# Performance work log

Hardware: AMD Instinct MI355X
Metric: run time of the kernel (lower is better)

Reference implementation:

```python
import jax, jax.numpy as jnp
import numpy as np

B, C_IN, C_OUT, H, W = 16, 32, 32, 256, 256
M1, M2 = 32, 32  # kept Fourier modes (kbase // 2**level)


def setup_inputs() -> dict:
    key = jax.random.key(0)
    ks = jax.random.split(key, 7)
    scale = 1.0 / (C_IN * C_OUT)
    return {
        "x": jax.random.normal(ks[0], (B, C_IN, H, W), dtype=jnp.float32),
        "conv_w": jax.random.normal(ks[1], (C_OUT, 3 * C_IN), dtype=jnp.float32) * (1.0 / np.sqrt(3 * C_IN)),
        "conv_b": jax.random.normal(ks[2], (C_OUT,), dtype=jnp.float32) * 0.01,
        "w1r": jax.random.normal(ks[3], (C_IN, C_OUT, M1, M2), dtype=jnp.float32) * scale,
        "w1i": jax.random.normal(ks[4], (C_IN, C_OUT, M1, M2), dtype=jnp.float32) * scale,
        "w2r": jax.random.normal(ks[5], (C_IN, C_OUT, M1, M2), dtype=jnp.float32) * scale,
        "w2i": jax.random.normal(ks[6], (C_IN, C_OUT, M1, M2), dtype=jnp.float32) * scale,
    }


def _combi_forward(x, conv_w, conv_b, w1r, w1i, w2r, w2i):
    # ---- diff branch: EasyDiffs (x, forward-diff along H, forward-diff along W) + 1x1 conv ----
    zrow = jnp.zeros_like(x[:, :, :1, :])
    zcol = jnp.zeros_like(x[:, :, :, :1])
    dh = jnp.concatenate([x[:, :, 1:, :] - x[:, :, :-1, :], zrow], axis=2)  # [B,C,H,W]
    dw = jnp.concatenate([x[:, :, :, 1:] - x[:, :, :, :-1], zcol], axis=3)  # [B,C,H,W]
    feats = jnp.concatenate([x, dh, dw], axis=1)  # [B,3C,H,W]
    diff_out = jnp.einsum("bchw,oc->bohw", feats, conv_w) + conv_b[None, :, None, None]

    # ---- spectral branch: rfft2 -> truncated complex multiply (two corners) -> irfft2 ----
    xf = jnp.fft.rfft2(x, axes=(-2, -1))  # [B,C,H,W//2+1] complex
    w1 = w1r + 1j * w1i
    w2 = w2r + 1j * w2i
    top = jnp.einsum("bixy,ioxy->boxy", xf[:, :, :M1, :M2], w1)
    bot = jnp.einsum("bixy,ioxy->boxy", xf[:, :, -M1:, :M2], w2)
    out_ft = jnp.zeros((B, C_OUT, H, W // 2 + 1), dtype=xf.dtype)
    out_ft = out_ft.at[:, :, :M1, :M2].set(top)
    out_ft = out_ft.at[:, :, -M1:, :M2].set(bot)
    fno_out = jnp.fft.irfft2(out_ft, s=(H, W), axes=(-2, -1))

    return diff_out + fno_out


def reference(x, conv_w, conv_b, w1r, w1i, w2r, w2i):
    return _combi_forward(x, conv_w, conv_b, w1r, w1i, w2r, w2i)
```

## Files before the change

### kernel.cpp

```cpp
#include <hip/hip_runtime.h>


#define PI2_256 0.02454369260617026f

__device__ __forceinline__ unsigned short bf16r(float f) {
    unsigned u = __float_as_uint(f);
    u += 0x7fffu + ((u >> 16) & 1u);
    return (unsigned short)(u >> 16);
}
__device__ __forceinline__ float bf16tof(unsigned short h) {
    return __uint_as_float((unsigned)h << 16);
}
__device__ __forceinline__ unsigned pack2(float a, float b) {
    return (unsigned)bf16r(a) | ((unsigned)bf16r(b) << 16);
}

typedef __attribute__((ext_vector_type(8))) short short8;
typedef __attribute__((ext_vector_type(4))) float float4v;

__global__ __launch_bounds__(256) void k_twiddle(float* __restrict__ ws) {
    unsigned short* E = (unsigned short*)(ws + 8388608);
    int idx0 = blockIdx.x * 256 + threadIdx.x;
    for (int idx = idx0; idx < 4 * 64 * 72; idx += 16 * 256) {
        int c = idx / 4608;
        int rem = idx - c * 4608;
        int col = rem / 72;
        int wp = rem - col * 72;
        unsigned short hi = 0, lo = 0;
        if (wp < 64) {
            int w = c * 64 + wp;
            int ky = col & 31;
            int prod = (ky * w) & 255;
            float s, cc;
            __sincosf(PI2_256 * (float)prod, &s, &cc);
            float val = (col < 32) ? cc : -s;
            hi = bf16r(val);
            lo = bf16r(val - bf16tof(hi));
        }
        E[c * 9216 + col * 72 + wp] = hi;
        E[c * 9216 + 4608 + col * 72 + wp] = lo;
    }
}

__global__ __launch_bounds__(256) void k_dftw(const float* __restrict__ x,
                                              const float* __restrict__ Ews,
                                              float* __restrict__ Ar,
                                              float* __restrict__ Ai) {
    __shared__ __align__(16) unsigned char smem[55296];
    unsigned short* Xhi = (unsigned short*)smem;
    unsigned short* Xlo = (unsigned short*)(smem + 18432);
    unsigned short* Ehi = (unsigned short*)(smem + 36864);
    float* obuf = (float*)smem;

    int t = threadIdx.x;
    int bc = blockIdx.x >> 1;
    int h0 = (blockIdx.x & 1) << 7;
    int lane = t & 63, wid = t >> 6;
    int quad = lane >> 4, col = lane & 15;

    const uint4* Ews4 = (const uint4*)Ews;

    float4v zero = {0.f, 0.f, 0.f, 0.f};
    float4v acc[4][2];
#pragma unroll
    for (int m = 0; m < 4; ++m) {
        acc[m][0] = zero;
        acc[m][1] = zero;
    }

    for (int c = 0; c < 4; ++c) {
        const float* xrow = x + ((size_t)bc * 256 + h0) * 256 + c * 64;
#pragma unroll
        for (int it = 0; it < 8; ++it) {
            int l = it * 256 + t;
            int r = l >> 4, f4 = l & 15;
            float4 v = *(const float4*)(xrow + (size_t)r * 256 + f4 * 4);
            unsigned short hx = bf16r(v.x), hy = bf16r(v.y);
            unsigned short hz = bf16r(v.z), hw = bf16r(v.w);
            unsigned hi0 = (unsigned)hx | ((unsigned)hy << 16);
            unsigned hi1 = (unsigned)hz | ((unsigned)hw << 16);
            unsigned lo0 = (unsigned)bf16r(v.x - bf16tof(hx)) |
                           ((unsigned)bf16r(v.y - bf16tof(hy)) << 16);
            unsigned lo1 = (unsigned)bf16r(v.z - bf16tof(hz)) |
                           ((unsigned)bf16r(v.w - bf16tof(hw)) << 16);
            int o = r * 72 + f4 * 4;
            *(uint2*)&Xhi[o] = make_uint2(hi0, hi1);
            *(uint2*)&Xlo[o] = make_uint2(lo0, lo1);
        }
        for (int g = t; g < 1152; g += 256)
            ((uint4*)(smem + 36864))[g] = Ews4[c * 1152 + g];
        __syncthreads();

#pragma unroll
        for (int ks = 0; ks < 2; ++ks) {
            int ko = quad * 8 + ks * 32;
            short8 ah[4], al[4], bh[2], bl[2];
#pragma unroll
            for (int m = 0; m < 4; ++m) {
                int ro = (m * 16 + col) * 72 + ko;
                ah[m] = *(const short8*)&Ehi[ro];
                al[m] = *(const short8*)&Ehi[4608 + ro];
            }
#pragma unroll
            for (int n = 0; n < 2; ++n) {
                int hr = ((wid * 2 + n) * 16 + col) * 72 + ko;
                bh[n] = *(const short8*)&Xhi[hr];
                bl[n] = *(const short8*)&Xlo[hr];
            }
#pragma unroll
            for (int m = 0; m < 4; ++m) {
#pragma unroll
                for (int n = 0; n < 2; ++n) {
                    acc[m][n] = __builtin_amdgcn_mfma_f32_16x16x32_bf16(ah[m], bh[n], acc[m][n], 0, 0, 0);
                    acc[m][n] = __builtin_amdgcn_mfma_f32_16x16x32_bf16(ah[m], bl[n], acc[m][n], 0, 0, 0);
                    acc[m][n] = __builtin_amdgcn_mfma_f32_16x16x32_bf16(al[m], bh[n], acc[m][n], 0, 0, 0);
                }
            }
        }
        __syncthreads();
    }

#pragma unroll
    for (int m = 0; m < 4; ++m) {
#pragma unroll
        for (int n = 0; n < 2; ++n) {
            int hl = (wid * 2 + n) * 16 + col;
            *(float4v*)&obuf[hl * 68 + m * 16 + quad * 4] = acc[m][n];
        }
    }
    __syncthreads();
#pragma unroll
    for (int it = 0; it < 8; ++it) {
        int l = it * 256 + t;
        int hh = l >> 4, f = l & 15;
        float4 v = *(float4*)&obuf[hh * 68 + f * 4];
        size_t g = (size_t)bc * 8192 + (size_t)(h0 + hh) * 32;
        if (f < 8) *(float4*)(Ar + g + f * 4) = v;
        else       *(float4*)(Ai + g + (f - 8) * 4) = v;
    }
}

#define DF_PITCH 72

__global__ __launch_bounds__(256) void k_dfth(const float* __restrict__ Ar,
                                              const float* __restrict__ Ai,
                                              float* __restrict__ xfr,
                                              float* __restrict__ xfi) {
    __shared__ __align__(16) unsigned short F2h[128 * DF_PITCH];
    __shared__ __align__(16) unsigned short F2l[128 * DF_PITCH];
    __shared__ __align__(16) unsigned short B2h[32 * DF_PITCH];
    __shared__ __align__(16) unsigned short B2l[32 * DF_PITCH];

    int t = threadIdx.x;
    int bc = blockIdx.x;
    int lane = t & 63, wid = t >> 6;
    int quad = lane >> 4, col = lane & 15;

    int m = t & 127;
    int kxi = m >> 1;
    int kx = (kxi < 32) ? kxi : kxi + 192;
    int neg = m & 1;
    int khalf = t >> 7;
    float c1, s1;
    __sincosf(PI2_256 * (float)kx, &s1, &c1);

    float4v zero = {0.f, 0.f, 0.f, 0.f};
    float4v acc[2][2];
    acc[0][0] = zero; acc[0][1] = zero; acc[1][0] = zero; acc[1][1] = zero;

    for (int hc = 0; hc < 8; ++hc) {
        {
            int h0 = hc * 32 + khalf * 16;
            float c, s;
            __sincosf(PI2_256 * (float)((kx * h0) & 255), &s, &c);
#pragma unroll
            for (int j = 0; j < 16; ++j) {
                int kk = 2 * (khalf * 16 + j);
                float ch = bf16tof(bf16r(c)), sh = bf16tof(bf16r(s));
                float cl = c - ch, sl = s - sh;
                unsigned hiw, low;
                if (neg == 0) { hiw = pack2(c, s);  low = pack2(cl, sl); }
                else          { hiw = pack2(-s, c); low = pack2(-sl, cl); }
                *(unsigned*)&F2h[m * DF_PITCH + kk] = hiw;
                *(unsigned*)&F2l[m * DF_PITCH + kk] = low;
                float nc = c * c1 - s * s1;
                s = s * c1 + c * s1;
                c = nc;
            }
        }
        {
            int hl = t >> 3;
            int ky0 = (t & 7) * 4;
            const float* pr = Ar + (size_t)bc * 8192 + (size_t)(hc * 32 + hl) * 32 + ky0;
            const float* pi = Ai + (size_t)bc * 8192 + (size_t)(hc * 32 + hl) * 32 + ky0;
            float4 vr = *(const float4*)pr;
            float4 vi = *(const float4*)pi;
            float fr[4] = {vr.x, vr.y, vr.z, vr.w};
            float fi[4] = {vi.x, vi.y, vi.z, vi.w};
#pragma unroll
            for (int q = 0; q < 4; ++q) {
                float ar = fr[q], ai = fi[q];
                float arh = bf16tof(bf16r(ar)), aih = bf16tof(bf16r(ai));
                *(unsigned*)&B2h[(ky0 + q) * DF_PITCH + 2 * hl] = pack2(ar, ai);
                *(unsigned*)&B2l[(ky0 + q) * DF_PITCH + 2 * hl] = pack2(ar - arh, ai - aih);
            }
        }
        __syncthreads();
#pragma unroll
        for (int ks = 0; ks < 2; ++ks) {
            int ko = ks * 32 + quad * 8;
            short8 ah[2], al[2], bh[2], bl[2];
#pragma unroll
            for (int mi = 0; mi < 2; ++mi) {
                int ro = ((wid * 2 + mi) * 16 + col) * DF_PITCH + ko;
                ah[mi] = *(const short8*)&F2h[ro];
                al[mi] = *(const short8*)&F2l[ro];
            }
#pragma unroll
            for (int ni = 0; ni < 2; ++ni) {
                int ro = (ni * 16 + col) * DF_PITCH + ko;
                bh[ni] = *(const short8*)&B2h[ro];
                bl[ni] = *(const short8*)&B2l[ro];
            }
#pragma unroll
            for (int mi = 0; mi < 2; ++mi) {
#pragma unroll
                for (int ni = 0; ni < 2; ++ni) {
                    acc[mi][ni] = __builtin_amdgcn_mfma_f32_16x16x32_bf16(ah[mi], bh[ni], acc[mi][ni], 0, 0, 0);
                    acc[mi][ni] = __builtin_amdgcn_mfma_f32_16x16x32_bf16(ah[mi], bl[ni], acc[mi][ni], 0, 0, 0);
                    acc[mi][ni] = __builtin_amdgcn_mfma_f32_16x16x32_bf16(al[mi], bh[ni], acc[mi][ni], 0, 0, 0);
                }
            }
        }
        __syncthreads();
    }
#pragma unroll
    for (int mi = 0; mi < 2; ++mi) {
#pragma unroll
        for (int ni = 0; ni < 2; ++ni) {
#pragma unroll
            for (int reg = 0; reg < 4; ++reg) {
                int mm = (wid * 2 + mi) * 16 + quad * 4 + reg;
                size_t g = (size_t)bc * 2048 + (size_t)(mm >> 1) * 32 + ni * 16 + col;
                if (mm & 1) xfi[g] = acc[mi][ni][reg];
                else        xfr[g] = acc[mi][ni][reg];
            }
        }
    }
}

__global__ __launch_bounds__(256) void k_mix(float* __restrict__ xfr,
                                             float* __restrict__ xfi,
                                             const float* __restrict__ w1r,
                                             const float* __restrict__ w1i,
                                             const float* __restrict__ w2r,
                                             const float* __restrict__ w2i) {
    __shared__ float wr[32 * 32 * 8];
    __shared__ float wi[32 * 32 * 8];
    __shared__ float xsr[32 * 8];
    __shared__ float xsi[32 * 8];
    int t = threadIdx.x;
    int kxi = (blockIdx.x >> 2) & 63;
    int ky0 = (blockIdx.x & 3) * 8;
    int b0 = (blockIdx.x >> 8) * 4;
    const float* Wr = (kxi < 32) ? w1r : w2r;
    const float* Wi = (kxi < 32) ? w1i : w2i;
    int m1 = kxi & 31;
#pragma unroll
    for (int it = 0; it < 32; ++it) {
        int l = it * 256 + t;
        int i = l >> 8, o = (l >> 3) & 31, q = l & 7;
        size_t g = (size_t)i * 32768 + (size_t)o * 1024 + m1 * 32 + ky0 + q;
        wr[l] = Wr[g];
        wi[l] = Wi[g];
    }
    __syncthreads();

    int o = t >> 3, q = t & 7;
    for (int b = b0; b < b0 + 4; ++b) {
        __syncthreads();
        {
            int i = t >> 3, qq = t & 7;
            size_t g = ((size_t)(b * 32 + i)) * 2048 + (size_t)kxi * 32 + ky0 + qq;
            xsr[t] = xfr[g];
            xsi[t] = xfi[g];
        }
        __syncthreads();
        float accr = 0.f, acci = 0.f;
#pragma unroll
        for (int i = 0; i < 32; ++i) {
            float xr = xsr[i * 8 + q], xim = xsi[i * 8 + q];
            float wrv = wr[i * 256 + o * 8 + q], wiv = wi[i * 256 + o * 8 + q];
            accr += xr * wrv - xim * wiv;
            acci += xr * wiv + xim * wrv;
        }
        size_t g = ((size_t)(b * 32 + o)) * 2048 + (size_t)kxi * 32 + ky0 + q;
        xfr[g] = accr;
        xfi[g] = acci;
    }
}

#define IF_PITCH 136

__global__ __launch_bounds__(256) void k_idfth(const float* __restrict__ ofr,
                                               const float* __restrict__ ofi,
                                               float* __restrict__ T) {
    __shared__ __align__(16) unsigned short Fh[64 * IF_PITCH];
    __shared__ __align__(16) unsigned short Fl[64 * IF_PITCH];
    __shared__ __align__(16) unsigned short Gh[64 * IF_PITCH];
    __shared__ __align__(16) unsigned short Gl[64 * IF_PITCH];

    int t = threadIdx.x;
    int bo = blockIdx.x;
    int lane = t & 63, wid = t >> 6;
    int quad = lane >> 4, col = lane & 15;

    {
        int kxi = t >> 2;
        int ky0 = (t & 3) * 8;
        const float* pr = ofr + (size_t)bo * 2048 + (size_t)kxi * 32 + ky0;
        const float* pi = ofi + (size_t)bo * 2048 + (size_t)kxi * 32 + ky0;
        float4 r0 = *(const float4*)pr, r1 = *(const float4*)(pr + 4);
        float4 i0 = *(const float4*)pi, i1 = *(const float4*)(pi + 4);
        float fr[8] = {r0.x, r0.y, r0.z, r0.w, r1.x, r1.y, r1.z, r1.w};
        float fi[8] = {i0.x, i0.y, i0.z, i0.w, i1.x, i1.y, i1.z, i1.w};
#pragma unroll
        for (int q = 0; q < 8; ++q) {
            int ky = ky0 + q;
            float sc = ((ky == 0) ? 1.f : 2.f) * (1.f / 65536.f);
            float vr = fr[q] * sc, vi = fi[q] * sc;
            float vrh = bf16tof(bf16r(vr)), vih = bf16tof(bf16r(vi));
            float vrl = vr - vrh, vil = vi - vih;
            *(unsigned*)&Gh[(2 * ky) * IF_PITCH + 2 * kxi]     = pack2(vr, -vi);
            *(unsigned*)&Gh[(2 * ky + 1) * IF_PITCH + 2 * kxi] = pack2(vi, vr);
            *(unsigned*)&Gl[(2 * ky) * IF_PITCH + 2 * kxi]     = pack2(vrl, -vil);
            *(unsigned*)&Gl[(2 * ky + 1) * IF_PITCH + 2 * kxi] = pack2(vil, vrl);
        }
    }

    int hl_ = t & 63;
    int g = t >> 6;
    int kxi0 = g * 16;
    int kx0 = (g < 2) ? kxi0 : kxi0 + 192;

    for (int hc = 0; hc < 4; ++hc) {
        int h = hc * 64 + hl_;
        {
            float c1, s1;
            __sincosf(PI2_256 * (float)h, &s1, &c1);
            float c, s;
            __sincosf(PI2_256 * (float)((kx0 * h) & 255), &s, &c);
#pragma unroll
            for (int j = 0; j < 16; ++j) {
                int kk = 2 * (kxi0 + j);
                float ch = bf16tof(bf16r(c)), sh = bf16tof(bf16r(s));
                *(unsigned*)&Fh[hl_ * IF_PITCH + kk] = pack2(c, s);
                *(unsigned*)&Fl[hl_ * IF_PITCH + kk] = pack2(c - ch, s - sh);
                float nc = c * c1 - s * s1;
                s = s * c1 + c * s1;
                c = nc;
            }
        }
        __syncthreads();
        float4v zero = {0.f, 0.f, 0.f, 0.f};
        float4v acc[4];
        acc[0] = zero; acc[1] = zero; acc[2] = zero; acc[3] = zero;
#pragma unroll
        for (int ks = 0; ks < 4; ++ks) {
            int ko = ks * 32 + quad * 8;
            short8 bh = *(const short8*)&Gh[(wid * 16 + col) * IF_PITCH + ko];
            short8 bl = *(const short8*)&Gl[(wid * 16 + col) * IF_PITCH + ko];
#pragma unroll
            for (int mt = 0; mt < 4; ++mt) {
                int ro = (mt * 16 + col) * IF_PITCH + ko;
                short8 ah = *(const short8*)&Fh[ro];
                short8 al = *(const short8*)&Fl[ro];
                acc[mt] = __builtin_amdgcn_mfma_f32_16x16x32_bf16(ah, bh, acc[mt], 0, 0, 0);
                acc[mt] = __builtin_amdgcn_mfma_f32_16x16x32_bf16(ah, bl, acc[mt], 0, 0, 0);
                acc[mt] = __builtin_amdgcn_mfma_f32_16x16x32_bf16(al, bh, acc[mt], 0, 0, 0);
            }
        }
        float* dst = T + (size_t)bo * 16384 + (size_t)hc * 4096;
#pragma unroll
        for (int mt = 0; mt < 4; ++mt) {
#pragma unroll
            for (int reg = 0; reg < 4; ++reg) {
                int hh = mt * 16 + quad * 4 + reg;
                dst[hh * 64 + wid * 16 + col] = acc[mt][reg];
            }
        }
        __syncthreads();
    }
}

#define BT_PITCH 164

__global__ __launch_bounds__(256) void k_final(const float* __restrict__ x,
                                               const float* __restrict__ cw,
                                               const float* __restrict__ cb,
                                               const float* __restrict__ T,
                                               float* __restrict__ out) {
    __shared__ unsigned short Bt[128 * BT_PITCH];
    __shared__ __align__(16) unsigned short Afr[5 * 2 * 64 * 8];

    int t = threadIdx.x;
    int b = blockIdx.x >> 9;
    int h = (blockIdx.x >> 1) & 255;
    int w0 = (blockIdx.x & 1) << 7;

    {
        int nn = t & 127, half = t >> 7;
        int w = w0 + nn;
        int hs = (h < 255) ? h + 1 : h;
        int we = (w < 255) ? 1 : 0;
#pragma unroll
        for (int ip = 0; ip < 8; ++ip) {
            int i0 = half * 16 + ip * 2;
            const float* x0 = x + ((size_t)(b * 32 + i0)) * 65536;
            const float* x1 = x0 + 65536;
            float c0 = x0[h * 256 + w];
            float s0 = x0[hs * 256 + w];
            float e0 = x0[h * 256 + w + we];
            float c1 = x1[h * 256 + w];
            float s1 = x1[hs * 256 + w];
            float e1 = x1[h * 256 + w + we];
            *(unsigned*)&Bt[nn * BT_PITCH + i0]      = pack2(c0, c1);
            *(unsigned*)&Bt[nn * BT_PITCH + 32 + i0] = pack2(s0 - c0, s1 - c1);
            *(unsigned*)&Bt[nn * BT_PITCH + 64 + i0] = pack2(e0 - c0, e1 - c1);
        }
    }
    {
        int nn = t & 127, half = t >> 7;
        int w = w0 + nn;
        float c1, s1;
        __sincosf(PI2_256 * (float)w, &s1, &c1);
        int kk0 = half * 16;
        float c, s;
        __sincosf(PI2_256 * (float)((w * kk0) & 255), &s, &c);
#pragma unroll
        for (int kp = 0; kp < 8; ++kp) {
            int kk = kk0 + kp * 2;
            float ca = c, sa = s;
            float nc = c * c1 - s * s1; s = s * c1 + c * s1; c = nc;
            float cbv = c, sbv = s;
            nc = c * c1 - s * s1; s = s * c1 + c * s1; c = nc;
            *(unsigned*)&Bt[nn * BT_PITCH + 96 + kk]  = pack2(ca, cbv);
            *(unsigned*)&Bt[nn * BT_PITCH + 128 + kk] = pack2(-sa, -sbv);
        }
    }
    for (int slot = t; slot < 640; slot += 256) {
        int ks = slot >> 7;
        int mt = (slot >> 6) & 1;
        int lane = slot & 63;
        int m = (lane & 15) + mt * 16;
        int kb = ks * 32 + (lane >> 4) * 8;
        float v[8];
        if (ks < 3) {
#pragma unroll
            for (int j = 0; j < 8; ++j) v[j] = cw[m * 96 + kb + j];
        } else {
            const float* tp = T + ((size_t)(b * 32 + m)) * 16384 + (size_t)h * 64;
            int kkb = kb - (ks == 3 ? 96 : 128);
            int im = (ks == 3) ? 0 : 1;
#pragma unroll
            for (int j = 0; j < 8; ++j) v[j] = tp[2 * (kkb + j) + im];
        }
        uint4 pk;
        pk.x = pack2(v[0], v[1]); pk.y = pack2(v[2], v[3]);
        pk.z = pack2(v[4], v[5]); pk.w = pack2(v[6], v[7]);
        *(uint4*)&Afr[((ks * 2 + mt) * 64 + lane) * 8] = pk;
    }
    __syncthreads();

    int lane = t & 63, wid = t >> 6;
    int quad = lane >> 4, col = lane & 15;
    float4v zero = {0.f, 0.f, 0.f, 0.f};
    float4v acc[2][2];
    acc[0][0] = zero; acc[0][1] = zero; acc[1][0] = zero; acc[1][1] = zero;

#pragma unroll
    for (int ks = 0; ks < 5; ++ks) {
        short8 a0 = *(const short8*)&Afr[((ks * 2 + 0) * 64 + lane) * 8];
        short8 a1 = *(const short8*)&Afr[((ks * 2 + 1) * 64 + lane) * 8];
        int kb = ks * 32 + quad * 8;
        union { unsigned long long q[2]; short8 v; } ub0, ub1;
        const unsigned short* r0 = &Bt[(wid * 32 + col) * BT_PITCH + kb];
        const unsigned short* r1 = &Bt[(wid * 32 + 16 + col) * BT_PITCH + kb];
        ub0.q[0] = *(const unsigned long long*)(r0);
        ub0.q[1] = *(const unsigned long long*)(r0 + 4);
        ub1.q[0] = *(const unsigned long long*)(r1);
        ub1.q[1] = *(const unsigned long long*)(r1 + 4);
        acc[0][0] = __builtin_amdgcn_mfma_f32_16x16x32_bf16(a0, ub0.v, acc[0][0], 0, 0, 0);
        acc[1][0] = __builtin_amdgcn_mfma_f32_16x16x32_bf16(a1, ub0.v, acc[1][0], 0, 0, 0);
        acc[0][1] = __builtin_amdgcn_mfma_f32_16x16x32_bf16(a0, ub1.v, acc[0][1], 0, 0, 0);
        acc[1][1] = __builtin_amdgcn_mfma_f32_16x16x32_bf16(a1, ub1.v, acc[1][1], 0, 0, 0);
    }

#pragma unroll
    for (int mt = 0; mt < 2; ++mt) {
#pragma unroll
        for (int nt = 0; nt < 2; ++nt) {
#pragma unroll
            for (int reg = 0; reg < 4; ++reg) {
                int o = mt * 16 + quad * 4 + reg;
                int w = w0 + wid * 32 + nt * 16 + col;
                out[(((size_t)(b * 32 + o)) * 256 + h) * 256 + w] = acc[mt][nt][reg] + cb[o];
            }
        }
    }
}

extern "C" void kernel_launch(void* const* d_in, const int* in_sizes, int n_in,
                              void* d_out, int out_size, void* d_ws, size_t ws_size,
                              hipStream_t stream) {
    const float* x = (const float*)d_in[0];
    const float* conv_w = (const float*)d_in[1];
    const float* conv_b = (const float*)d_in[2];
    const float* w1r = (const float*)d_in[3];
    const float* w1i = (const float*)d_in[4];
    const float* w2r = (const float*)d_in[5];
    const float* w2i = (const float*)d_in[6];
    float* out = (float*)d_out;

    float* ws = (float*)d_ws;
    float* Ar = ws;
    float* Ai = ws + 4194304;
    float* Tbuf = ws;
    float* xfr = ws + 8388608;
    float* xfi = ws + 9437184;
    const float* Ews = ws + 8388608;

    k_twiddle<<<16, 256, 0, stream>>>(ws);
    k_dftw<<<1024, 256, 0, stream>>>(x, Ews, Ar, Ai);
    k_dfth<<<512, 256, 0, stream>>>(Ar, Ai, xfr, xfi);
    k_mix<<<1024, 256, 0, stream>>>(xfr, xfi, w1r, w1i, w2r, w2i);
    k_idfth<<<512, 256, 0, stream>>>(xfr, xfi, Tbuf);
    k_final<<<8192, 256, 0, stream>>>(x, conv_w, conv_b, Tbuf, out);
}
```

Measured before the change: 431.8 us.

## Precompute bf16 twiddle and conv-weight fragments, store intermediate as bf16

A new small kernel precomputes the bf16 W-direction twiddle table and the conv weights packed in MFMA fragment order. k_idfth now writes its output as bf16, with rows reordered so k_final can load A fragments directly from global memory into registers. k_final no longer runs sincos per block and writes B operands in fragment-native LDS layout, which removes the padded pitch and the split 64-bit loads. The aim is to cut per-block setup work, halve intermediate traffic, and shrink LDS to raise occupancy, at some cost in precision on the spectral term.

```diff
diff --git a/kernel.cpp b/kernel.cpp
--- a/kernel.cpp
+++ b/kernel.cpp
@@ -42,6 +42,24 @@
     }
 }
 
+__global__ __launch_bounds__(256) void k_tables(const float* __restrict__ cw,
+                                                float* __restrict__ ws) {
+    unsigned short* TWt = (unsigned short*)(ws + 6291456);
+    unsigned short* CWf = (unsigned short*)(ws + 6301696);
+    int id = blockIdx.x * 256 + threadIdx.x;
+    int w = id >> 6, kk = id & 63;
+    float s, c;
+    __sincosf(PI2_256 * (float)(((kk & 31) * w) & 255), &s, &c);
+    TWt[id] = bf16r(kk < 32 ? c : -s);
+    if (id < 3072) {
+        int j = id & 7, slot = id >> 3;
+        int ks = slot >> 7, mt = (slot >> 6) & 1, lane = slot & 63;
+        int m = (lane & 15) + mt * 16;
+        int kb = ks * 32 + ((lane >> 4) & 3) * 8;
+        CWf[id] = bf16r(cw[m * 96 + kb + j]);
+    }
+}
+
 __global__ __launch_bounds__(256) void k_dftw(const float* __restrict__ x,
                                               const float* __restrict__ Ews,
                                               float* __restrict__ Ar,
@@ -304,7 +322,7 @@
 
 __global__ __launch_bounds__(256) void k_idfth(const float* __restrict__ ofr,
                                                const float* __restrict__ ofi,
-                                               float* __restrict__ T) {
+                                               unsigned short* __restrict__ T2) {
     __shared__ __align__(16) unsigned short Fh[64 * IF_PITCH];
     __shared__ __align__(16) unsigned short Fl[64 * IF_PITCH];
     __shared__ __align__(16) unsigned short Gh[64 * IF_PITCH];
@@ -331,10 +349,10 @@
             float vr = fr[q] * sc, vi = fi[q] * sc;
             float vrh = bf16tof(bf16r(vr)), vih = bf16tof(bf16r(vi));
             float vrl = vr - vrh, vil = vi - vih;
-            *(unsigned*)&Gh[(2 * ky) * IF_PITCH + 2 * kxi]     = pack2(vr, -vi);
-            *(unsigned*)&Gh[(2 * ky + 1) * IF_PITCH + 2 * kxi] = pack2(vi, vr);
-            *(unsigned*)&Gl[(2 * ky) * IF_PITCH + 2 * kxi]     = pack2(vrl, -vil);
-            *(unsigned*)&Gl[(2 * ky + 1) * IF_PITCH + 2 * kxi] = pack2(vil, vrl);
+            *(unsigned*)&Gh[ky * IF_PITCH + 2 * kxi]        = pack2(vr, -vi);
+            *(unsigned*)&Gh[(32 + ky) * IF_PITCH + 2 * kxi] = pack2(vi, vr);
+            *(unsigned*)&Gl[ky * IF_PITCH + 2 * kxi]        = pack2(vrl, -vil);
+            *(unsigned*)&Gl[(32 + ky) * IF_PITCH + 2 * kxi] = pack2(vil, vrl);
         }
     }
 
@@ -380,120 +398,99 @@
                 acc[mt] = __builtin_amdgcn_mfma_f32_16x16x32_bf16(al, bh, acc[mt], 0, 0, 0);
             }
         }
-        float* dst = T + (size_t)bo * 16384 + (size_t)hc * 4096;
+        unsigned short* dst = T2 + (size_t)bo * 16384 + (size_t)hc * 64 * 64;
+        int n = wid * 16 + col;
 #pragma unroll
         for (int mt = 0; mt < 4; ++mt) {
 #pragma unroll
             for (int reg = 0; reg < 4; ++reg) {
                 int hh = mt * 16 + quad * 4 + reg;
-                dst[hh * 64 + wid * 16 + col] = acc[mt][reg];
-            }
-        }
-        __syncthreads();
-    }
-}
-
-#define BT_PITCH 164
-
-__global__ __launch_bounds__(256) void k_final(const float* __restrict__ x,
-                                               const float* __restrict__ cw,
-                                               const float* __restrict__ cb,
-                                               const float* __restrict__ T,
-                                               float* __restrict__ out) {
-    __shared__ unsigned short Bt[128 * BT_PITCH];
-    __shared__ __align__(16) unsigned short Afr[5 * 2 * 64 * 8];
+                dst[hh * 64 + n] = bf16r(acc[mt][reg]);
+            }
+        }
+        __syncthreads();
+    }
+}
+
+__global__ __launch_bounds__(256, 4) void k_final(const float* __restrict__ x,
+                                                  const unsigned short* __restrict__ cwf,
+                                                  const unsigned short* __restrict__ TWt,
+                                                  const float* __restrict__ cb,
+                                                  const unsigned short* __restrict__ T2,
+                                                  float* __restrict__ out) {
+    __shared__ __align__(16) unsigned short Bf[5 * 8 * 64 * 8];
 
     int t = threadIdx.x;
     int b = blockIdx.x >> 9;
     int h = (blockIdx.x >> 1) & 255;
     int w0 = (blockIdx.x & 1) << 7;
-
-    {
-        int nn = t & 127, half = t >> 7;
-        int w = w0 + nn;
-        int hs = (h < 255) ? h + 1 : h;
-        int we = (w < 255) ? 1 : 0;
-#pragma unroll
-        for (int ip = 0; ip < 8; ++ip) {
-            int i0 = half * 16 + ip * 2;
-            const float* x0 = x + ((size_t)(b * 32 + i0)) * 65536;
-            const float* x1 = x0 + 65536;
-            float c0 = x0[h * 256 + w];
-            float s0 = x0[hs * 256 + w];
-            float e0 = x0[h * 256 + w + we];
-            float c1 = x1[h * 256 + w];
-            float s1 = x1[hs * 256 + w];
-            float e1 = x1[h * 256 + w + we];
-            *(unsigned*)&Bt[nn * BT_PITCH + i0]      = pack2(c0, c1);
-            *(unsigned*)&Bt[nn * BT_PITCH + 32 + i0] = pack2(s0 - c0, s1 - c1);
-            *(unsigned*)&Bt[nn * BT_PITCH + 64 + i0] = pack2(e0 - c0, e1 - c1);
-        }
-    }
-    {
-        int nn = t & 127, half = t >> 7;
-        int w = w0 + nn;
-        float c1, s1;
-        __sincosf(PI2_256 * (float)w, &s1, &c1);
-        int kk0 = half * 16;
-        float c, s;
-        __sincosf(PI2_256 * (float)((w * kk0) & 255), &s, &c);
-#pragma unroll
-        for (int kp = 0; kp < 8; ++kp) {
-            int kk = kk0 + kp * 2;
-            float ca = c, sa = s;
-            float nc = c * c1 - s * s1; s = s * c1 + c * s1; c = nc;
-            float cbv = c, sbv = s;
-            nc = c * c1 - s * s1; s = s * c1 + c * s1; c = nc;
-            *(unsigned*)&Bt[nn * BT_PITCH + 96 + kk]  = pack2(ca, cbv);
-            *(unsigned*)&Bt[nn * BT_PITCH + 128 + kk] = pack2(-sa, -sbv);
-        }
-    }
-    for (int slot = t; slot < 640; slot += 256) {
-        int ks = slot >> 7;
-        int mt = (slot >> 6) & 1;
-        int lane = slot & 63;
-        int m = (lane & 15) + mt * 16;
-        int kb = ks * 32 + (lane >> 4) * 8;
-        float v[8];
-        if (ks < 3) {
-#pragma unroll
-            for (int j = 0; j < 8; ++j) v[j] = cw[m * 96 + kb + j];
-        } else {
-            const float* tp = T + ((size_t)(b * 32 + m)) * 16384 + (size_t)h * 64;
-            int kkb = kb - (ks == 3 ? 96 : 128);
-            int im = (ks == 3) ? 0 : 1;
-#pragma unroll
-            for (int j = 0; j < 8; ++j) v[j] = tp[2 * (kkb + j) + im];
-        }
-        uint4 pk;
-        pk.x = pack2(v[0], v[1]); pk.y = pack2(v[2], v[3]);
-        pk.z = pack2(v[4], v[5]); pk.w = pack2(v[6], v[7]);
-        *(uint4*)&Afr[((ks * 2 + mt) * 64 + lane) * 8] = pk;
-    }
-    __syncthreads();
-
     int lane = t & 63, wid = t >> 6;
     int quad = lane >> 4, col = lane & 15;
+
+    short8 a[5][2];
+#pragma unroll
+    for (int ks = 0; ks < 3; ++ks)
+#pragma unroll
+        for (int mt = 0; mt < 2; ++mt)
+            a[ks][mt] = *(const short8*)&cwf[((ks * 2 + mt) * 64 + lane) * 8];
+#pragma unroll
+    for (int ks = 3; ks < 5; ++ks)
+#pragma unroll
+        for (int mt = 0; mt < 2; ++mt) {
+            int m = (lane & 15) + mt * 16;
+            a[ks][mt] = *(const short8*)&T2[((size_t)(b * 32 + m) * 256 + h) * 64
+                                            + (ks - 3) * 32 + quad * 8];
+        }
+
+    int nn = t & 127, half = t >> 7;
+    int w = w0 + nn;
+    int wt = nn >> 4, colw = nn & 15;
+    int hs = (h < 255) ? h + 1 : h;
+    int we = (w < 255) ? 1 : 0;
+#pragma unroll
+    for (int ip = 0; ip < 2; ++ip) {
+        int i0 = half * 16 + ip * 8;
+        float c[8], sv[8], ev[8];
+#pragma unroll
+        for (int j = 0; j < 8; ++j) {
+            const float* xp = x + ((size_t)(b * 32 + i0 + j)) * 65536;
+            c[j]  = xp[h * 256 + w];
+            sv[j] = xp[hs * 256 + w];
+            ev[j] = xp[h * 256 + w + we];
+        }
+        uint4 pc, ps, pe;
+        pc.x = pack2(c[0], c[1]); pc.y = pack2(c[2], c[3]);
+        pc.z = pack2(c[4], c[5]); pc.w = pack2(c[6], c[7]);
+        ps.x = pack2(sv[0] - c[0], sv[1] - c[1]); ps.y = pack2(sv[2] - c[2], sv[3] - c[3]);
+        ps.z = pack2(sv[4] - c[4], sv[5] - c[5]); ps.w = pack2(sv[6] - c[6], sv[7] - c[7]);
+        pe.x = pack2(ev[0] - c[0], ev[1] - c[1]); pe.y = pack2(ev[2] - c[2], ev[3] - c[3]);
+        pe.z = pack2(ev[4] - c[4], ev[5] - c[5]); pe.w = pack2(ev[6] - c[6], ev[7] - c[7]);
+        int qp = half * 2 + ip;
+        *(uint4*)&Bf[((0 * 8 + wt) * 64 + qp * 16 + colw) * 8] = pc;
+        *(uint4*)&Bf[((1 * 8 + wt) * 64 + qp * 16 + colw) * 8] = ps;
+        *(uint4*)&Bf[((2 * 8 + wt) * 64 + qp * 16 + colw) * 8] = pe;
+    }
+    {
+        const uint4* tw = (const uint4*)&TWt[w * 64 + half * 32];
+#pragma unroll
+        for (int q = 0; q < 4; ++q) {
+            uint4 v = tw[q];
+            *(uint4*)&Bf[(((3 + half) * 8 + wt) * 64 + q * 16 + colw) * 8] = v;
+        }
+    }
+    __syncthreads();
+
     float4v zero = {0.f, 0.f, 0.f, 0.f};
     float4v acc[2][2];
     acc[0][0] = zero; acc[0][1] = zero; acc[1][0] = zero; acc[1][1] = zero;
-
 #pragma unroll
     for (int ks = 0; ks < 5; ++ks) {
-        short8 a0 = *(const short8*)&Afr[((ks * 2 + 0) * 64 + lane) * 8];
-        short8 a1 = *(const short8*)&Afr[((ks * 2 + 1) * 64 + lane) * 8];
-        int kb = ks * 32 + quad * 8;
-        union { unsigned long long q[2]; short8 v; } ub0, ub1;
-        const unsigned short* r0 = &Bt[(wid * 32 + col) * BT_PITCH + kb];
-        const unsigned short* r1 = &Bt[(wid * 32 + 16 + col) * BT_PITCH + kb];
-        ub0.q[0] = *(const unsigned long long*)(r0);
-        ub0.q[1] = *(const unsigned long long*)(r0 + 4);
-        ub1.q[0] = *(const unsigned long long*)(r1);
-        ub1.q[1] = *(const unsigned long long*)(r1 + 4);
-        acc[0][0] = __builtin_amdgcn_mfma_f32_16x16x32_bf16(a0, ub0.v, acc[0][0], 0, 0, 0);
-        acc[1][0] = __builtin_amdgcn_mfma_f32_16x16x32_bf16(a1, ub0.v, acc[1][0], 0, 0, 0);
-        acc[0][1] = __builtin_amdgcn_mfma_f32_16x16x32_bf16(a0, ub1.v, acc[0][1], 0, 0, 0);
-        acc[1][1] = __builtin_amdgcn_mfma_f32_16x16x32_bf16(a1, ub1.v, acc[1][1], 0, 0, 0);
+#pragma unroll
+        for (int nt = 0; nt < 2; ++nt) {
+            short8 ub = *(const short8*)&Bf[((ks * 8 + wid * 2 + nt) * 64 + lane) * 8];
+            acc[0][nt] = __builtin_amdgcn_mfma_f32_16x16x32_bf16(a[ks][0], ub, acc[0][nt], 0, 0, 0);
+            acc[1][nt] = __builtin_amdgcn_mfma_f32_16x16x32_bf16(a[ks][1], ub, acc[1][nt], 0, 0, 0);
+        }
     }
 
 #pragma unroll
@@ -503,8 +500,8 @@
 #pragma unroll
             for (int reg = 0; reg < 4; ++reg) {
                 int o = mt * 16 + quad * 4 + reg;
-                int w = w0 + wid * 32 + nt * 16 + col;
-                out[(((size_t)(b * 32 + o)) * 256 + h) * 256 + w] = acc[mt][nt][reg] + cb[o];
+                int ww = w0 + wid * 32 + nt * 16 + col;
+                out[(((size_t)(b * 32 + o)) * 256 + h) * 256 + ww] = acc[mt][nt][reg] + cb[o];
             }
         }
     }
@@ -525,15 +522,18 @@
     float* ws = (float*)d_ws;
     float* Ar = ws;
     float* Ai = ws + 4194304;
-    float* Tbuf = ws;
+    unsigned short* T2 = (unsigned short*)ws;
     float* xfr = ws + 8388608;
     float* xfi = ws + 9437184;
     const float* Ews = ws + 8388608;
+    const unsigned short* TWt = (const unsigned short*)(ws + 6291456);
+    const unsigned short* CWf = (const unsigned short*)(ws + 6301696);
 
     k_twiddle<<<16, 256, 0, stream>>>(ws);
     k_dftw<<<1024, 256, 0, stream>>>(x, Ews, Ar, Ai);
     k_dfth<<<512, 256, 0, stream>>>(Ar, Ai, xfr, xfi);
+    k_tables<<<64, 256, 0, stream>>>(conv_w, ws);
     k_mix<<<1024, 256, 0, stream>>>(xfr, xfi, w1r, w1i, w2r, w2i);
-    k_idfth<<<512, 256, 0, stream>>>(xfr, xfi, Tbuf);
-    k_final<<<8192, 256, 0, stream>>>(x, conv_w, conv_b, Tbuf, out);
-}
+    k_idfth<<<512, 256, 0, stream>>>(xfr, xfi, T2);
+    k_final<<<8192, 256, 0, stream>>>(x, CWf, TWt, conv_b, T2, out);
+}
```

Result: no change. 427.9 us (-0.9%).
